# Performance work log

Measured on AMD Instinct MI355X. Metric: run time of the kernel, lower is better.

Reference implementation:

```python
import jax, jax.numpy as jnp
import numpy as np
from jax import lax

H, W, K, B = 64, 64, 64, 64
OFFSETS = [(0, 1), (2, 1), (1, 0), (1, 2)]  # up, down, left, right slices into padded grid


def setup_inputs() -> dict:
    key = jax.random.key(0)
    ks = jax.random.split(key, 7)
    n = H * W * 3
    s = lambda d: 1.0 / np.sqrt(d)
    return {
        "obs_flat": jax.random.normal(ks[0], (B, n), jnp.float32),
        "phi_w": jax.random.normal(ks[1], (n, n), jnp.float32) * s(n),
        "phi_b": jax.random.normal(ks[2], (n,), jnp.float32) * s(n),
        "w1": jax.random.normal(ks[3], (36, 16), jnp.float32) * s(36),
        "b1": jax.random.normal(ks[4], (16,), jnp.float32) * s(36),
        "w2": jax.random.normal(ks[5], (16, 4), jnp.float32) * s(16),
        "b2": jax.random.normal(ks[6], (4,), jnp.float32) * s(16),
    }


def _vin(rin, rout, p):
    # rin, rout, p: [B, H, W]. K Bellman-style 4-neighbor sweeps.
    prin = jnp.pad(rin, ((0, 0), (1, 1), (1, 1)))
    rin_sh = jnp.stack([prin[:, ho:ho + H, wo:wo + W] for ho, wo in OFFSETS])  # [4,B,H,W]
    rout_masked = rout[None] * (rin_sh != 0).astype(rin.dtype)                 # [4,B,H,W]

    def step(V, _):
        pv = jnp.pad(V, ((0, 0), (1, 1), (1, 1)))
        v_sh = jnp.stack([pv[:, ho:ho + H, wo:wo + W] for ho, wo in OFFSETS])
        nv = p[None] * v_sh + rin_sh - rout_masked
        return jnp.maximum(V, nv.max(axis=0)), None

    V0 = jnp.zeros_like(rin)
    V, _ = lax.scan(step, V0, None, length=K)
    return V


def reference(obs_flat, phi_w, phi_b, w1, b1, w2, b2):
    obs = obs_flat.reshape(B, H, W, 3)
    phi = (obs_flat @ phi_w + phi_b).reshape(B, H, W, 3)
    rin, rout = phi[..., 0], phi[..., 1]
    p = jax.nn.softmax(phi[..., 2].reshape(B, H * W), axis=1).reshape(B, H, W)

    V = _vin(rin, rout, p)  # [B,H,W]
    obs_val = jnp.concatenate([obs, V[..., None]], axis=-1)  # [B,H,W,4]
    padded = jnp.pad(obs_val, ((0, 0), (1, 1), (1, 1), (0, 0)))

    # agent position = location of the (one-hot) nonzero in channel 1
    flat = jnp.argmax(obs[..., 1].reshape(B, -1), axis=1)
    pi, pj = flat // W, flat % W
    patch = jax.vmap(lambda x, i, j: lax.dynamic_slice(x, (i, j, 0), (3, 3, 4)))(padded, pi, pj)

    h = jax.nn.relu(patch.reshape(B, 36) @ w1 + b1)
    logit = h @ w2 + b2  # [B, 4]
    return logit
```

## Files before the change

### kernel.cpp

```cpp
#include <hip/hip_runtime.h>
#include <hip/hip_bf16.h>

typedef __attribute__((ext_vector_type(8))) short short8;
typedef __attribute__((ext_vector_type(4))) float floatx4;
typedef __attribute__((ext_vector_type(4))) unsigned short ushort4v;
typedef __attribute__((ext_vector_type(8))) unsigned short ushort8v;

#define N_DIM 12288
#define SPLITK 4
#define KCHUNK (N_DIM / SPLITK)
#define KSTEP 64
#define KITERS (KCHUNK / KSTEP)
#define NTILE 64

__device__ __forceinline__ unsigned short f2bf(float f) {
  union { float f; unsigned int i; } x; x.f = f;
  unsigned int r = x.i + 0x7fffu + ((x.i >> 16) & 1u);
  return (unsigned short)(r >> 16);
}

__global__ __launch_bounds__(256) void gemm_phi(
    const float* __restrict__ obs, const float* __restrict__ W,
    const float* __restrict__ bias, float* __restrict__ phi_part)
{
  __shared__ unsigned short A_s[2][64 * 72];
  __shared__ unsigned short W_s[2][64 * 72];

  const int t = threadIdx.x;
  const int n0 = blockIdx.x * NTILE;
  const int s  = blockIdx.y;
  const int k0 = s * KCHUNK;
  const int lane = t & 63, wv = t >> 6;
  const int l16 = lane & 15, q = lane >> 4;
  const int m0f = 16 * wv;

  const int am = t >> 2, akq = (t & 3) * 16;
  const int rg = t >> 4, cg = t & 15;

  const float* aptr = obs + (size_t)am * N_DIM + k0 + akq;
  const float* wptr = W + (size_t)(k0 + 4 * rg) * N_DIM + (n0 + 4 * cg);

  floatx4 pa0, pa1, pa2, pa3, pw0, pw1, pw2, pw3;
  floatx4 qa0, qa1, qa2, qa3, qw0, qw1, qw2, qw3;

#define LOADS(A0, A1, A2, A3, W0, W1, W2, W3, TI) do {                       \
    const float* ap_ = aptr + (TI) * KSTEP;                                  \
    const float* wp_ = wptr + (size_t)(TI) * KSTEP * N_DIM;                  \
    A0 = *(const floatx4*)(ap_);       A1 = *(const floatx4*)(ap_ + 4);      \
    A2 = *(const floatx4*)(ap_ + 8);   A3 = *(const floatx4*)(ap_ + 12);     \
    W0 = *(const floatx4*)(wp_);               W1 = *(const floatx4*)(wp_ + N_DIM);     \
    W2 = *(const floatx4*)(wp_ + 2 * N_DIM);   W3 = *(const floatx4*)(wp_ + 3 * N_DIM); \
  } while (0)

  LOADS(pa0, pa1, pa2, pa3, pw0, pw1, pw2, pw3, 0);
  LOADS(qa0, qa1, qa2, qa3, qw0, qw1, qw2, qw3, 1);

  floatx4 acc[4];
#pragma unroll
  for (int i = 0; i < 4; i++) acc[i] = (floatx4){0.f, 0.f, 0.f, 0.f};

#define STEP(TI, A0, A1, A2, A3, W0, W1, W2, W3, BUF, LAST) do {             \
    if (LAST) asm volatile("s_waitcnt vmcnt(0)" ::: "memory");               \
    else      asm volatile("s_waitcnt vmcnt(8)" ::: "memory");               \
    {                                          \
      ushort8v u0, u1;                                                       \
      _Pragma("unroll")                                                      \
      for (int i = 0; i < 4; i++) {                                          \
        u0[i] = f2bf(A0[i]); u0[4 + i] = f2bf(A1[i]);                        \
        u1[i] = f2bf(A2[i]); u1[4 + i] = f2bf(A3[i]);                        \
      }                                                                      \
      *(ushort8v*)&A_s[BUF][am * 72 + akq]     = u0;                         \
      *(ushort8v*)&A_s[BUF][am * 72 + akq + 8] = u1;                         \
      _Pragma("unroll")                                                      \
      for (int i = 0; i < 4; i++) {                                          \
        ushort4v v = { f2bf(W0[i]), f2bf(W1[i]), f2bf(W2[i]), f2bf(W3[i]) }; \
        *(ushort4v*)&W_s[BUF][(4 * cg + i) * 72 + 4 * rg] = v;               \
      }                                                                      \
    }                                                                        \
    if ((TI) + 2 < KITERS) {      \
      LOADS(A0, A1, A2, A3, W0, W1, W2, W3, (TI) + 2);                       \
    }                                                                        \
    asm volatile("s_waitcnt lgkmcnt(0)" ::: "memory");   \
    __builtin_amdgcn_s_barrier();                                            \
    __builtin_amdgcn_sched_barrier(0);                                       \
    _Pragma("unroll")                                                        \
    for (int kk = 0; kk < 2; ++kk) {                                         \
      short8 af = *(const short8*)&A_s[BUF][(m0f + l16) * 72 + 32 * kk + 8 * q]; \
      _Pragma("unroll")                                                      \
      for (int nt = 0; nt < 4; ++nt) {                                       \
        short8 wf = *(const short8*)&W_s[BUF][(16 * nt + l16) * 72 + 32 * kk + 8 * q]; \
        acc[nt] = __builtin_amdgcn_mfma_f32_16x16x32_bf16(af, wf, acc[nt], 0, 0, 0); \
      }                                                                      \
    }                                                                        \
  } while (0)

  for (int it2 = 0; it2 < KITERS; it2 += 2) {
    STEP(it2,     pa0, pa1, pa2, pa3, pw0, pw1, pw2, pw3, 0, false);
    STEP(it2 + 1, qa0, qa1, qa2, qa3, qw0, qw1, qw2, qw3, 1, (it2 + 1 == KITERS - 1));
  }

  float* dst = phi_part + (size_t)s * 64 * N_DIM;
#pragma unroll
  for (int nt = 0; nt < 4; ++nt) {
    const int ncol = n0 + 16 * nt + l16;
    const float bv = (s == 0) ? bias[ncol] : 0.f;
#pragma unroll
    for (int r = 0; r < 4; ++r) {
      const int m = m0f + q * 4 + r;
      dst[(size_t)m * N_DIM + ncol] = acc[nt][r] + bv;
    }
  }
#undef STEP
#undef LOADS
}

#define VSTR 76
#define VOFF(h, w) (((h) + 1) * VSTR + (w) + 4)

__global__ __launch_bounds__(256) void vin_mlp(
    const float* __restrict__ obs, const float* __restrict__ phi,
    const float* __restrict__ w1, const float* __restrict__ b1,
    const float* __restrict__ w2, const float* __restrict__ b2,
    float* __restrict__ out)
{
  __shared__ float Vb[2][66 * VSTR];
  __shared__ float red_v[256];
  __shared__ int   red_i[256];

  const int b = blockIdx.x;
  const int t = threadIdx.x;
  const int ty = t >> 4, tx = t & 15;
  const int h0 = ty * 4, w0 = tx * 4;

  for (int i = t; i < 2 * 66 * VSTR; i += 256) (&Vb[0][0])[i] = 0.f;

  float rin[16], rout[16], lg[16];
#pragma unroll
  for (int r = 0; r < 4; r++) {
    const int j = 3 * ((h0 + r) * 64 + w0);
    const float* base = phi + (size_t)b * N_DIM + j;
    floatx4 x0 = *(const floatx4*)(base);
    floatx4 x1 = *(const floatx4*)(base + 4);
    floatx4 x2 = *(const floatx4*)(base + 8);
#pragma unroll
    for (int sp = 1; sp < SPLITK; sp++) {
      const float* bs = base + (size_t)sp * 64 * N_DIM;
      x0 += *(const floatx4*)(bs);
      x1 += *(const floatx4*)(bs + 4);
      x2 += *(const floatx4*)(bs + 8);
    }
    float f[12];
#pragma unroll
    for (int c = 0; c < 4; c++) { f[c] = x0[c]; f[4 + c] = x1[c]; f[8 + c] = x2[c]; }
#pragma unroll
    for (int c = 0; c < 4; c++) {
      rin [r * 4 + c] = f[3 * c + 0];
      rout[r * 4 + c] = f[3 * c + 1];
      lg  [r * 4 + c] = f[3 * c + 2];
    }
  }

  float lmax = -3.4e38f;
#pragma unroll
  for (int i = 0; i < 16; i++) lmax = fmaxf(lmax, lg[i]);
  __syncthreads();
  red_v[t] = lmax; __syncthreads();
  for (int o = 128; o > 0; o >>= 1) { if (t < o) red_v[t] = fmaxf(red_v[t], red_v[t + o]); __syncthreads(); }
  const float M = red_v[0];
  __syncthreads();
  float p[16]; float esum = 0.f;
#pragma unroll
  for (int i = 0; i < 16; i++) { p[i] = __expf(lg[i] - M); esum += p[i]; }
  red_v[t] = esum; __syncthreads();
  for (int o = 128; o > 0; o >>= 1) { if (t < o) red_v[t] += red_v[t + o]; __syncthreads(); }
  const float inv = 1.f / red_v[0];
  __syncthreads();
#pragma unroll
  for (int i = 0; i < 16; i++) p[i] *= inv;

#pragma unroll
  for (int r = 0; r < 4; r++) {
    floatx4 rr = { rin[r * 4 + 0], rin[r * 4 + 1], rin[r * 4 + 2], rin[r * 4 + 3] };
    *(floatx4*)&Vb[1][VOFF(h0 + r, w0)] = rr;
  }
  __syncthreads();
  float cu[16], cdn[16], cl[16], cr[16];
#pragma unroll
  for (int r = 0; r < 4; r++) {
#pragma unroll
    for (int c = 0; c < 4; c++) {
      const int i = r * 4 + c, h = h0 + r, w = w0 + c;
      const float nu = Vb[1][VOFF(h - 1, w)];
      const float nd = Vb[1][VOFF(h + 1, w)];
      const float nl = Vb[1][VOFF(h, w - 1)];
      const float nr = Vb[1][VOFF(h, w + 1)];
      cu [i] = nu - (nu != 0.f ? rout[i] : 0.f);
      cdn[i] = nd - (nd != 0.f ? rout[i] : 0.f);
      cl [i] = nl - (nl != 0.f ? rout[i] : 0.f);
      cr [i] = nr - (nr != 0.f ? rout[i] : 0.f);
    }
  }
  __syncthreads();

  float v[16];
#pragma unroll
  for (int i = 0; i < 16; i++) v[i] = 0.f;

  for (int k = 0; k < 64; k++) {
    const float* Vc = Vb[k & 1];
    float* Vn = Vb[(k & 1) ^ 1];
    const floatx4 top = *(const floatx4*)&Vc[VOFF(h0 - 1, w0)];
    const floatx4 bot = *(const floatx4*)&Vc[VOFF(h0 + 4, w0)];
    float lf[4], rt[4];
#pragma unroll
    for (int r = 0; r < 4; r++) { lf[r] = Vc[VOFF(h0 + r, w0 - 1)]; rt[r] = Vc[VOFF(h0 + r, w0 + 4)]; }
    float nv[16];
#pragma unroll
    for (int r = 0; r < 4; r++) {
#pragma unroll
      for (int c = 0; c < 4; c++) {
        const int i = r * 4 + c;
        const float vu = (r == 0) ? top[c] : v[i - 4];
        const float vd = (r == 3) ? bot[c] : v[i + 4];
        const float vl = (c == 0) ? lf[r] : v[i - 1];
        const float vr = (c == 3) ? rt[r] : v[i + 1];
        const float m1 = fmaxf(fmaf(p[i], vu, cu[i]), fmaf(p[i], vd, cdn[i]));
        const float m2 = fmaxf(fmaf(p[i], vl, cl[i]), fmaf(p[i], vr, cr[i]));
        nv[i] = fmaxf(v[i], fmaxf(m1, m2));
      }
    }
#pragma unroll
    for (int r = 0; r < 4; r++) {
      floatx4 w4 = { nv[r * 4 + 0], nv[r * 4 + 1], nv[r * 4 + 2], nv[r * 4 + 3] };
      *(floatx4*)&Vn[VOFF(h0 + r, w0)] = w4;
    }
#pragma unroll
    for (int i = 0; i < 16; i++) v[i] = nv[i];
    __syncthreads();
  }

  float amax = -3.4e38f; int aidx = 0;
#pragma unroll
  for (int r = 0; r < 4; r++) {
#pragma unroll
    for (int c = 0; c < 4; c++) {
      const int cell = (h0 + r) * 64 + (w0 + c);
      const float val = obs[(size_t)b * N_DIM + 3 * cell + 1];
      if (val > amax) { amax = val; aidx = cell; }
    }
  }
  red_v[t] = amax; red_i[t] = aidx;
  __syncthreads();
  for (int o = 128; o > 0; o >>= 1) {
    if (t < o) {
      const float v2 = red_v[t + o]; const int i2 = red_i[t + o];
      if (v2 > red_v[t] || (v2 == red_v[t] && i2 < red_i[t])) { red_v[t] = v2; red_i[t] = i2; }
    }
    __syncthreads();
  }
  const int pos = red_i[0];
  const int pi = pos >> 6, pj = pos & 63;
  __syncthreads();

  if (t < 36) {
    const int di = t / 12, rem = t % 12, dj = rem / 4, c4 = rem & 3;
    const int hh = pi - 1 + di, ww = pj - 1 + dj;
    float pv;
    if (c4 < 3) {
      pv = (hh >= 0 && hh < 64 && ww >= 0 && ww < 64)
           ? obs[(size_t)b * N_DIM + 3 * (hh * 64 + ww) + c4] : 0.f;
    } else {
      pv = Vb[0][VOFF(hh, ww)];
    }
    red_v[t] = pv;
  }
  __syncthreads();
  if (t < 16) {
    float a = b1[t];
#pragma unroll
    for (int j = 0; j < 36; j++) a = fmaf(red_v[j], w1[j * 16 + t], a);
    red_v[64 + t] = fmaxf(a, 0.f);
  }
  __syncthreads();
  if (t < 4) {
    float a = b2[t];
#pragma unroll
    for (int i = 0; i < 16; i++) a = fmaf(red_v[64 + i], w2[i * 4 + t], a);
    out[b * 4 + t] = a;
  }
}

extern "C" void kernel_launch(void* const* d_in, const int* in_sizes, int n_in,
                              void* d_out, int out_size, void* d_ws, size_t ws_size,
                              hipStream_t stream)
{
  (void)in_sizes; (void)n_in; (void)out_size; (void)ws_size;
  const float* obs  = (const float*)d_in[0];
  const float* phiw = (const float*)d_in[1];
  const float* phib = (const float*)d_in[2];
  const float* w1   = (const float*)d_in[3];
  const float* b1   = (const float*)d_in[4];
  const float* w2   = (const float*)d_in[5];
  const float* b2   = (const float*)d_in[6];
  float* phi = (float*)d_ws;
  float* out = (float*)d_out;

  hipLaunchKernelGGL(gemm_phi, dim3(N_DIM / NTILE, SPLITK), dim3(256), 0, stream,
                     obs, phiw, phib, phi);
  hipLaunchKernelGGL(vin_mlp, dim3(64), dim3(256), 0, stream,
                     obs, phi, w1, b1, w2, b2, out);
}
```

Baseline: 819.6 us.

## Retile phi GEMM to 256-wide tiles with split-K 16 and separate reduce kernel

Reshapes the phi GEMM into 512-thread blocks with 256-column tiles, KSTEP 32 and split-K 16. This raises the block count to 48x16, and W is now loaded one column per lane so global reads coalesce. LDS drops to a single buffer with two barriers per step, and a new reduce_phi kernel sums the 16 partial slabs so vin_mlp reads a single reduced phi. The aim is better occupancy and memory efficiency on the bandwidth-bound W stream, paid for with a larger partial-sum workspace, an extra launch and less load/compute overlap.

Result: no change. 815.8 us (-0.5%).

```diff
diff --git a/kernel.cpp b/kernel.cpp
--- a/kernel.cpp
+++ b/kernel.cpp
@@ -7,11 +7,12 @@
 typedef __attribute__((ext_vector_type(8))) unsigned short ushort8v;
 
 #define N_DIM 12288
-#define SPLITK 4
+#define SPLITK 16
 #define KCHUNK (N_DIM / SPLITK)
-#define KSTEP 64
+#define KSTEP 32
 #define KITERS (KCHUNK / KSTEP)
-#define NTILE 64
+#define NTILE 256
+#define WSTR 40
 
 __device__ __forceinline__ unsigned short f2bf(float f) {
   union { float f; unsigned int i; } x; x.f = f;
@@ -19,12 +20,12 @@
   return (unsigned short)(r >> 16);
 }
 
-__global__ __launch_bounds__(256) void gemm_phi(
+__global__ __launch_bounds__(512) void gemm_phi(
     const float* __restrict__ obs, const float* __restrict__ W,
     const float* __restrict__ bias, float* __restrict__ phi_part)
 {
-  __shared__ unsigned short A_s[2][64 * 72];
-  __shared__ unsigned short W_s[2][64 * 72];
+  __shared__ unsigned short A_s[64 * WSTR];
+  __shared__ unsigned short W_s[NTILE * WSTR];
 
   const int t = threadIdx.x;
   const int n0 = blockIdx.x * NTILE;
@@ -32,86 +33,92 @@
   const int k0 = s * KCHUNK;
   const int lane = t & 63, wv = t >> 6;
   const int l16 = lane & 15, q = lane >> 4;
-  const int m0f = 16 * wv;
-
-  const int am = t >> 2, akq = (t & 3) * 16;
-  const int rg = t >> 4, cg = t & 15;
-
-  const float* aptr = obs + (size_t)am * N_DIM + k0 + akq;
-  const float* wptr = W + (size_t)(k0 + 4 * rg) * N_DIM + (n0 + 4 * cg);
-
-  floatx4 pa0, pa1, pa2, pa3, pw0, pw1, pw2, pw3;
-  floatx4 qa0, qa1, qa2, qa3, qw0, qw1, qw2, qw3;
-
-#define LOADS(A0, A1, A2, A3, W0, W1, W2, W3, TI) do {                       \
-    const float* ap_ = aptr + (TI) * KSTEP;                                  \
-    const float* wp_ = wptr + (size_t)(TI) * KSTEP * N_DIM;                  \
-    A0 = *(const floatx4*)(ap_);       A1 = *(const floatx4*)(ap_ + 4);      \
-    A2 = *(const floatx4*)(ap_ + 8);   A3 = *(const floatx4*)(ap_ + 12);     \
-    W0 = *(const floatx4*)(wp_);               W1 = *(const floatx4*)(wp_ + N_DIM);     \
-    W2 = *(const floatx4*)(wp_ + 2 * N_DIM);   W3 = *(const floatx4*)(wp_ + 3 * N_DIM); \
+  const int wm = wv & 3, wn = wv >> 2;
+
+  const int am = t >> 3, ac = (t & 7) * 4;
+  const float* aptr = obs + (size_t)am * N_DIM + k0 + ac;
+
+  const int wn_idx = 64 * (wv & 3) + lane;
+  const int wkg    = (wv >> 2) * 16;
+  const float* wptr = W + (size_t)(k0 + wkg) * N_DIM + (n0 + wn_idx);
+
+  floatx4 pa, qa;
+  float pw[16], qw[16];
+
+#define LOADS(AV, WA, TI) do {                                               \
+    AV = *(const floatx4*)(aptr + (size_t)(TI) * KSTEP);                     \
+    _Pragma("unroll")                                                        \
+    for (int j = 0; j < 16; ++j)                                             \
+      WA[j] = wptr[(size_t)((TI) * KSTEP + j) * N_DIM];                      \
   } while (0)
 
-  LOADS(pa0, pa1, pa2, pa3, pw0, pw1, pw2, pw3, 0);
-  LOADS(qa0, qa1, qa2, qa3, qw0, qw1, qw2, qw3, 1);
-
-  floatx4 acc[4];
-#pragma unroll
-  for (int i = 0; i < 4; i++) acc[i] = (floatx4){0.f, 0.f, 0.f, 0.f};
-
-#define STEP(TI, A0, A1, A2, A3, W0, W1, W2, W3, BUF, LAST) do {             \
-    if (LAST) asm volatile("s_waitcnt vmcnt(0)" ::: "memory");               \
-    else      asm volatile("s_waitcnt vmcnt(8)" ::: "memory");               \
-    {                                          \
-      ushort8v u0, u1;                                                       \
-      _Pragma("unroll")                                                      \
-      for (int i = 0; i < 4; i++) {                                          \
-        u0[i] = f2bf(A0[i]); u0[4 + i] = f2bf(A1[i]);                        \
-        u1[i] = f2bf(A2[i]); u1[4 + i] = f2bf(A3[i]);                        \
-      }                                                                      \
-      *(ushort8v*)&A_s[BUF][am * 72 + akq]     = u0;                         \
-      *(ushort8v*)&A_s[BUF][am * 72 + akq + 8] = u1;                         \
-      _Pragma("unroll")                                                      \
-      for (int i = 0; i < 4; i++) {                                          \
-        ushort4v v = { f2bf(W0[i]), f2bf(W1[i]), f2bf(W2[i]), f2bf(W3[i]) }; \
-        *(ushort4v*)&W_s[BUF][(4 * cg + i) * 72 + 4 * rg] = v;               \
-      }                                                                      \
-    }                                                                        \
-    if ((TI) + 2 < KITERS) {      \
-      LOADS(A0, A1, A2, A3, W0, W1, W2, W3, (TI) + 2);                       \
-    }                                                                        \
-    asm volatile("s_waitcnt lgkmcnt(0)" ::: "memory");   \
+#define CONVSTORE(AV, WA) do {                                               \
+    ushort4v ua = { f2bf(AV[0]), f2bf(AV[1]), f2bf(AV[2]), f2bf(AV[3]) };    \
+    *(ushort4v*)&A_s[am * WSTR + ac] = ua;                                   \
+    ushort8v u0, u1;                                                         \
+    _Pragma("unroll")                                                        \
+    for (int j = 0; j < 8; ++j) { u0[j] = f2bf(WA[j]); u1[j] = f2bf(WA[8 + j]); } \
+    *(ushort8v*)&W_s[wn_idx * WSTR + wkg]     = u0;                          \
+    *(ushort8v*)&W_s[wn_idx * WSTR + wkg + 8] = u1;                          \
+  } while (0)
+
+  LOADS(pa, pw, 0);
+  LOADS(qa, qw, 1);
+
+  floatx4 acc[8];
+#pragma unroll
+  for (int i = 0; i < 8; i++) acc[i] = (floatx4){0.f, 0.f, 0.f, 0.f};
+
+#define STEP(TI, AV, WA) do {                                                \
+    CONVSTORE(AV, WA);              \
+    if ((TI) + 2 < KITERS) LOADS(AV, WA, (TI) + 2);                          \
+    asm volatile("s_waitcnt lgkmcnt(0)" ::: "memory");                       \
     __builtin_amdgcn_s_barrier();                                            \
     __builtin_amdgcn_sched_barrier(0);                                       \
-    _Pragma("unroll")                                                        \
-    for (int kk = 0; kk < 2; ++kk) {                                         \
-      short8 af = *(const short8*)&A_s[BUF][(m0f + l16) * 72 + 32 * kk + 8 * q]; \
+    {                                                                        \
+      short8 af = *(const short8*)&A_s[(16 * wm + l16) * WSTR + 8 * q];      \
       _Pragma("unroll")                                                      \
-      for (int nt = 0; nt < 4; ++nt) {                                       \
-        short8 wf = *(const short8*)&W_s[BUF][(16 * nt + l16) * 72 + 32 * kk + 8 * q]; \
+      for (int nt = 0; nt < 8; ++nt) {                                       \
+        short8 wf = *(const short8*)&W_s[(128 * wn + 16 * nt + l16) * WSTR + 8 * q]; \
         acc[nt] = __builtin_amdgcn_mfma_f32_16x16x32_bf16(af, wf, acc[nt], 0, 0, 0); \
       }                                                                      \
     }                                                                        \
+    asm volatile("s_waitcnt lgkmcnt(0)" ::: "memory");                       \
+    __builtin_amdgcn_s_barrier();    \
+    __builtin_amdgcn_sched_barrier(0);                                       \
   } while (0)
 
-  for (int it2 = 0; it2 < KITERS; it2 += 2) {
-    STEP(it2,     pa0, pa1, pa2, pa3, pw0, pw1, pw2, pw3, 0, false);
-    STEP(it2 + 1, qa0, qa1, qa2, qa3, qw0, qw1, qw2, qw3, 1, (it2 + 1 == KITERS - 1));
+  for (int it = 0; it < KITERS; it += 2) {
+    STEP(it,     pa, pw);
+    STEP(it + 1, qa, qw);
   }
 
   float* dst = phi_part + (size_t)s * 64 * N_DIM;
 #pragma unroll
-  for (int nt = 0; nt < 4; ++nt) {
-    const int ncol = n0 + 16 * nt + l16;
+  for (int nt = 0; nt < 8; ++nt) {
+    const int ncol = n0 + 128 * wn + 16 * nt + l16;
     const float bv = (s == 0) ? bias[ncol] : 0.f;
 #pragma unroll
     for (int r = 0; r < 4; ++r) {
-      const int m = m0f + q * 4 + r;
+      const int m = 16 * wm + q * 4 + r;
       dst[(size_t)m * N_DIM + ncol] = acc[nt][r] + bv;
     }
   }
 #undef STEP
+#undef CONVSTORE
 #undef LOADS
+}
+
+__global__ __launch_bounds__(256) void reduce_phi(
+    const float* __restrict__ part, float* __restrict__ sum)
+{
+  const size_t g = (size_t)blockIdx.x * 256 + threadIdx.x;
+  const float* p = part + 4 * g;
+  floatx4 a = *(const floatx4*)(p);
+#pragma unroll
+  for (int sp = 1; sp < SPLITK; ++sp)
+    a += *(const floatx4*)(p + (size_t)sp * 64 * N_DIM);
+  *(floatx4*)(sum + 4 * g) = a;
 }
 
 #define VSTR 76
@@ -138,17 +145,8 @@
 #pragma unroll
   for (int r = 0; r < 4; r++) {
     const int j = 3 * ((h0 + r) * 64 + w0);
-    const float* base = phi + (size_t)b * N_DIM + j;
-    floatx4 x0 = *(const floatx4*)(base);
-    floatx4 x1 = *(const floatx4*)(base + 4);
-    floatx4 x2 = *(const floatx4*)(base + 8);
-#pragma unroll
-    for (int sp = 1; sp < SPLITK; sp++) {
-      const float* bs = base + (size_t)sp * 64 * N_DIM;
-      x0 += *(const floatx4*)(bs);
-      x1 += *(const floatx4*)(bs + 4);
-      x2 += *(const floatx4*)(bs + 8);
-    }
+    const floatx4* p4 = (const floatx4*)(phi + (size_t)b * N_DIM + j);
+    floatx4 x0 = p4[0], x1 = p4[1], x2 = p4[2];
     float f[12];
 #pragma unroll
     for (int c = 0; c < 4; c++) { f[c] = x0[c]; f[4 + c] = x1[c]; f[8 + c] = x2[c]; }
@@ -302,11 +300,14 @@
   const float* b1   = (const float*)d_in[4];
   const float* w2   = (const float*)d_in[5];
   const float* b2   = (const float*)d_in[6];
-  float* phi = (float*)d_ws;
+  float* phi_part = (float*)d_ws;
+  float* phi_sum  = phi_part + (size_t)SPLITK * 64 * N_DIM;
   float* out = (float*)d_out;
 
-  hipLaunchKernelGGL(gemm_phi, dim3(N_DIM / NTILE, SPLITK), dim3(256), 0, stream,
-                     obs, phiw, phib, phi);
+  hipLaunchKernelGGL(gemm_phi, dim3(N_DIM / NTILE, SPLITK), dim3(512), 0, stream,
+                     obs, phiw, phib, phi_part);
+  hipLaunchKernelGGL(reduce_phi, dim3(64 * N_DIM / 4 / 256), dim3(256), 0, stream,
+                     phi_part, phi_sum);
   hipLaunchKernelGGL(vin_mlp, dim3(64), dim3(256), 0, stream,
-                     obs, phi, w1, b1, w2, b2, out);
-}
+                     obs, phi_sum, w1, b1, w2, b2, out);
+}
```
